# Kernel optimization log

Hardware: AMD Instinct MI355X
Metric: run time of the kernel (lower is better)

## Reference

```python
import jax, jax.numpy as jnp
import numpy as np

N = 100000
E = 1600000
D_IN = 50
D_H = 128
D_OUT = 128
EPS = 1e-5


def setup_inputs() -> dict:
    key = jax.random.key(0)
    ks = jax.random.split(key, 24)
    def w(k, shape, fan_in):
        return jax.random.normal(k, shape, jnp.float32) / np.sqrt(fan_in)
    inp = {
        'x': jax.random.normal(ks[0], (N, D_IN), jnp.float32),
        'edge_src': jax.random.randint(ks[1], (E,), 0, N, jnp.int32),
        'edge_dst': jax.random.randint(ks[2], (E,), 0, N, jnp.int32),
        # SAGEConv 1: D_IN -> D_H
        'Wl1': w(ks[3], (D_IN, D_H), D_IN), 'Wr1': w(ks[4], (D_IN, D_H), D_IN), 'b1': jnp.zeros((D_H,), jnp.float32),
        # SAGEConv 2: D_H -> D_H
        'Wl2': w(ks[5], (D_H, D_H), D_H), 'Wr2': w(ks[6], (D_H, D_H), D_H), 'b2': jnp.zeros((D_H,), jnp.float32),
        # SAGEConv 3: D_H -> D_OUT
        'Wl3': w(ks[7], (D_H, D_OUT), D_H), 'Wr3': w(ks[8], (D_H, D_OUT), D_H), 'b3': jnp.zeros((D_OUT,), jnp.float32),
        # skip linears (no bias)
        'Ws1': w(ks[9], (D_IN, D_H), D_IN), 'Ws2': w(ks[10], (D_IN, D_H), D_IN),
        # LayerNorm affine
        'lnw1': jnp.ones((D_H,), jnp.float32), 'lnb1': jnp.zeros((D_H,), jnp.float32),
        'lnw2': jnp.ones((D_H,), jnp.float32), 'lnb2': jnp.zeros((D_H,), jnp.float32),
        'lnw3': jnp.ones((D_OUT,), jnp.float32), 'lnb3': jnp.zeros((D_OUT,), jnp.float32),
        # PReLU scalar slopes (PyG init 0.25)
        'a1': jnp.float32(0.25), 'a2': jnp.float32(0.25), 'a3': jnp.float32(0.25),
    }
    return inp


def _sage(x, src, dst, Wl, Wr, b):
    # mean aggregation of source features at destinations, then linear + root
    msg = x[src]                                              # [E, d]
    agg = jax.ops.segment_sum(msg, dst, num_segments=N)       # [N, d]
    cnt = jax.ops.segment_sum(jnp.ones((src.shape[0],), x.dtype), dst, num_segments=N)
    mean = agg / jnp.maximum(cnt, 1.0)[:, None]
    return mean @ Wl + x @ Wr + b


def _graph_ln(x, w, b):
    # PyG LayerNorm mode='graph', batch=None: normalize over all nodes+channels
    xc = x - jnp.mean(x)
    std = jnp.sqrt(jnp.mean(xc * xc))
    return (xc / (std + EPS)) * w + b


def _prelu(x, a):
    return jnp.where(x >= 0, x, a * x)


def reference(x, edge_src, edge_dst, Wl1, Wr1, b1, Wl2, Wr2, b2, Wl3, Wr3, b3,
              Ws1, Ws2, lnw1, lnb1, lnw2, lnb2, lnw3, lnb3, a1, a2, a3):
    h1 = _sage(x, edge_src, edge_dst, Wl1, Wr1, b1)
    h1 = _prelu(_graph_ln(h1, lnw1, lnb1), a1)
    h2 = _sage(h1 + x @ Ws1, edge_src, edge_dst, Wl2, Wr2, b2)
    h2 = _prelu(_graph_ln(h2, lnw2, lnb2), a2)
    ret = _sage(h1 + h2 + x @ Ws2, edge_src, edge_dst, Wl3, Wr3, b3)
    ret = _prelu(_graph_ln(ret, lnw3, lnb3), a3)
    return ret
```

## Files before the change

kernel.cpp:

```cpp
#include <hip/hip_runtime.h>

#define D_IN 50
#define LN_EPS 1e-5f
#define BSH 8
#define MAXB 512

typedef __bf16 bf16_t;
typedef bf16_t bf16x8 __attribute__((ext_vector_type(8)));
typedef bf16_t bf16x4 __attribute__((ext_vector_type(4)));
typedef bf16_t bf16x2 __attribute__((ext_vector_type(2)));
typedef float f32x4_t __attribute__((ext_vector_type(4)));
typedef float f32x2_t __attribute__((ext_vector_type(2)));

#define ACCP(r, A)                                                            \
    {                                                                         \
        A[0] += (f32x2_t){__uint_as_float((r).x << 16),                       \
                          __uint_as_float((r).x & 0xffff0000u)};              \
        A[1] += (f32x2_t){__uint_as_float((r).y << 16),                       \
                          __uint_as_float((r).y & 0xffff0000u)};              \
        A[2] += (f32x2_t){__uint_as_float((r).z << 16),                       \
                          __uint_as_float((r).z & 0xffff0000u)};              \
        A[3] += (f32x2_t){__uint_as_float((r).w << 16),                       \
                          __uint_as_float((r).w & 0xffff0000u)};              \
    }

__global__ void bucket_hist_k(const int* __restrict__ dst, int* __restrict__ bcnt,
                              int e, int nb) {
    __shared__ int lh[MAXB];
    int t = threadIdx.x;
    for (int i = t; i < nb; i += 256) lh[i] = 0;
    __syncthreads();
    for (int i = blockIdx.x * 256 + t; i < e; i += gridDim.x * 256)
        atomicAdd(&lh[dst[i] >> BSH], 1);
    __syncthreads();
    for (int i = t; i < nb; i += 256) {
        int c = lh[i];
        if (c) atomicAdd(&bcnt[i * 16], c);
    }
}

__global__ void bscan_k(const int* __restrict__ bcnt, int* __restrict__ boff,
                        int* __restrict__ bpos, int nb, int e) {
    __shared__ int l[MAXB];
    int t = threadIdx.x;
    l[t] = (t < nb) ? bcnt[t * 16] : 0;
    __syncthreads();
    for (int off = 1; off < MAXB; off <<= 1) {
        int v = (t >= off) ? l[t - off] : 0;
        __syncthreads();
        l[t] += v;
        __syncthreads();
    }
    int excl = (t > 0) ? l[t - 1] : 0;
    if (t < nb) { boff[t] = excl; bpos[t * 16] = excl; }
    if (t == 0) boff[nb] = e;
}

__global__ void scatter_k(const int* __restrict__ src, const int* __restrict__ dst,
                          int* __restrict__ bpos, unsigned* __restrict__ pool,
                          int e, int nb) {
    __shared__ int lh[MAXB];
    __shared__ int lcur[MAXB];
    int t = threadIdx.x;
    for (int i = t; i < nb; i += 256) lh[i] = 0;
    __syncthreads();
    int chunk = (e + gridDim.x - 1) / gridDim.x;
    int s = blockIdx.x * chunk;
    int en = min(e, s + chunk);
    for (int i = s + t; i < en; i += 256)
        atomicAdd(&lh[dst[i] >> BSH], 1);
    __syncthreads();
    for (int i = t; i < nb; i += 256) {
        int c = lh[i];
        lcur[i] = c ? atomicAdd(&bpos[i * 16], c) : 0;
    }
    __syncthreads();
    for (int i = s + t; i < en; i += 256) {
        int d = dst[i];
        int p = atomicAdd(&lcur[d >> BSH], 1);
        pool[p] = (unsigned)src[i] | ((unsigned)(d & 255) << 17);
    }
}

__global__ void nhist_cfill_k(const unsigned* __restrict__ pool, const int* __restrict__ boff,
                              int* __restrict__ rp, int* __restrict__ col, int n) {
    __shared__ int lc[256];
    __shared__ int ls[256];
    __shared__ int lpos[256];
    int b = blockIdx.x, t = threadIdx.x;
    lc[t] = 0;
    __syncthreads();
    int s = boff[b], e = boff[b + 1];
    for (int i = s + t; i < e; i += 256) atomicAdd(&lc[pool[i] >> 17], 1);
    __syncthreads();
    int v = lc[t];
    ls[t] = v;
    __syncthreads();
    for (int off = 1; off < 256; off <<= 1) {
        int x = (t >= off) ? ls[t - off] : 0;
        __syncthreads();
        ls[t] += x;
        __syncthreads();
    }
    int excl = ls[t] - v;
    int nd = (b << BSH) + t;
    if (nd < n) rp[nd] = s + excl;
    if (nd == n - 1) rp[n] = e;
    lpos[t] = s + excl;
    __syncthreads();
    for (int i = s + t; i < e; i += 256) {
        unsigned pk = pool[i];
        int slot = atomicAdd(&lpos[pk >> 17], 1);
        col[slot] = (int)(pk & 0x1FFFFu);
    }
}

struct ConvDesc { const float* w; bf16_t* o; int kin; int kpad; };
struct ConvArgs { ConvDesc d[8]; };

__global__ void conv_w_k(ConvArgs args) {
    ConvDesc d = args.d[blockIdx.y];
    int i = blockIdx.x * 256 + threadIdx.x;
    int tot = 128 * d.kpad;
    if (i >= tot) return;
    int n = i / d.kpad, k = i - n * d.kpad;
    float v = (k < d.kin) ? d.w[(size_t)k * 128 + n] : 0.f;
    d.o[i] = (bf16_t)v;
}

__global__ void conv_x_k(const float* __restrict__ x, bf16_t* __restrict__ xb, int n) {
    int i = blockIdx.x * 256 + threadIdx.x;
    if (i >= n * 64) return;
    int node = i >> 6, k = i & 63;
    xb[i] = (k < D_IN) ? (bf16_t)x[node * D_IN + k] : (bf16_t)0.f;
}

__global__ void agg_bf64_k(const bf16_t* __restrict__ feat, const int* __restrict__ rp,
                           const int* __restrict__ col, bf16_t* __restrict__ mean, int n) {
    int wid = (blockIdx.x * blockDim.x + threadIdx.x) >> 6;
    int lane = threadIdx.x & 63;
    if (wid >= n) return;
    int start = rp[wid], end = rp[wid + 1];
    int lc = lane & 7;
    int g = lane >> 3;
    f32x2_t accA[4], accB[4];
#pragma unroll
    for (int k = 0; k < 4; k++) { accA[k] = (f32x2_t){0.f, 0.f}; accB[k] = (f32x2_t){0.f, 0.f}; }
    int e = start + g;
    if (e + 8 < end) {
        int i0 = col[e], i1 = col[e + 8];
        for (; e + 24 < end; e += 16) {
            uint4 r0 = *(const uint4*)(feat + (size_t)i0 * 64 + lc * 8);
            uint4 r1 = *(const uint4*)(feat + (size_t)i1 * 64 + lc * 8);
            i0 = col[e + 16];
            i1 = col[e + 24];
            ACCP(r0, accA);
            ACCP(r1, accB);
        }
        uint4 r0 = *(const uint4*)(feat + (size_t)i0 * 64 + lc * 8);
        uint4 r1 = *(const uint4*)(feat + (size_t)i1 * 64 + lc * 8);
        ACCP(r0, accA);
        ACCP(r1, accB);
        e += 16;
    }
    for (; e < end; e += 8) {
        uint4 r0 = *(const uint4*)(feat + (size_t)col[e] * 64 + lc * 8);
        ACCP(r0, accA);
    }
#pragma unroll
    for (int k = 0; k < 4; k++) accA[k] += accB[k];
    float aL[4], aH[4];
#pragma unroll
    for (int k = 0; k < 4; k++) { aL[k] = accA[k].x; aH[k] = accA[k].y; }
#pragma unroll
    for (int off = 8; off < 64; off <<= 1) {
#pragma unroll
        for (int k = 0; k < 4; k++) {
            aL[k] += __shfl_xor(aL[k], off);
            aH[k] += __shfl_xor(aH[k], off);
        }
    }
    int c = end - start;
    float invc = 1.f / (float)(c > 0 ? c : 1);
    if (lane < 8) {
        bf16x8 o;
#pragma unroll
        for (int k = 0; k < 4; k++) {
            o[2 * k] = (bf16_t)(aL[k] * invc);
            o[2 * k + 1] = (bf16_t)(aH[k] * invc);
        }
        *(bf16x8*)(mean + (size_t)wid * 64 + lc * 8) = o;
    }
}

__global__ void agg_bf128_k(const bf16_t* __restrict__ feat, const int* __restrict__ rp,
                            const int* __restrict__ col, bf16_t* __restrict__ mean, int n) {
    int wid = (blockIdx.x * blockDim.x + threadIdx.x) >> 6;
    int lane = threadIdx.x & 63;
    if (wid >= n) return;
    int start = rp[wid], end = rp[wid + 1];
    int lc = lane & 15;
    int g = lane >> 4;
    const uint* fp = (const uint*)feat + lc * 4;
    f32x2_t accA[4], accB[4];
#pragma unroll
    for (int k = 0; k < 4; k++) { accA[k] = (f32x2_t){0.f, 0.f}; accB[k] = (f32x2_t){0.f, 0.f}; }
    int e = start + g;
    int ng = (e < end) ? (((end - 1 - e) >> 2) + 1) : 0;
    int it = 0;
    for (; it + 4 <= ng; it += 4, e += 16) {
        int a = col[e], b = col[e + 4], c = col[e + 8], d = col[e + 12];
        uint4 r0 = *(const uint4*)(fp + (size_t)a * 64);
        uint4 r1 = *(const uint4*)(fp + (size_t)b * 64);
        uint4 r2 = *(const uint4*)(fp + (size_t)c * 64);
        uint4 r3 = *(const uint4*)(fp + (size_t)d * 64);
        ACCP(r0, accA);
        ACCP(r1, accB);
        ACCP(r2, accA);
        ACCP(r3, accB);
    }
    int rem = ng - it;
    if (rem > 0) {
        int a = col[e];
        int b = (rem > 1) ? col[e + 4] : a;
        int c = (rem > 2) ? col[e + 8] : b;
        uint4 r0 = *(const uint4*)(fp + (size_t)a * 64);
        uint4 r1 = *(const uint4*)(fp + (size_t)b * 64);
        uint4 r2 = *(const uint4*)(fp + (size_t)c * 64);
        ACCP(r0, accA);
        if (rem > 1) ACCP(r1, accB);
        if (rem > 2) ACCP(r2, accA);
    }
#pragma unroll
    for (int k = 0; k < 4; k++) accA[k] += accB[k];
    float aL[4], aH[4];
#pragma unroll
    for (int k = 0; k < 4; k++) { aL[k] = accA[k].x; aH[k] = accA[k].y; }
#pragma unroll
    for (int off = 16; off < 64; off <<= 1) {
#pragma unroll
        for (int k = 0; k < 4; k++) {
            aL[k] += __shfl_xor(aL[k], off);
            aH[k] += __shfl_xor(aH[k], off);
        }
    }
    int c = end - start;
    float invc = 1.f / (float)(c > 0 ? c : 1);
    if (lane < 16) {
        bf16x8 o;
#pragma unroll
        for (int k = 0; k < 4; k++) {
            o[2 * k] = (bf16_t)(aL[k] * invc);
            o[2 * k + 1] = (bf16_t)(aH[k] * invc);
        }
        *(bf16x8*)(mean + (size_t)wid * 128 + lc * 8) = o;
    }
}

template <int KPAD, bool DUAL, bool ACC>
__global__ __launch_bounds__(256) void mfma_gemm_k(
    const bf16_t* __restrict__ A, const bf16_t* __restrict__ B,
    const bf16_t* __restrict__ WlT, const bf16_t* __restrict__ WrT,
    const float* __restrict__ bias,
    bf16_t* __restrict__ out, float2* __restrict__ partials, int M) {
    constexpr int KC = KPAD / 32;
    constexpr int WELE = 8 * KC * 64 * 8;
    __shared__ bf16_t lwl[WELE];
    __shared__ bf16_t lwr[DUAL ? WELE : 8];

    const int tid = threadIdx.x;
    for (int ch = tid; ch < 8 * KC * 64; ch += 256) {
        int nt = ch / (KC * 64);
        int rem = ch - nt * (KC * 64);
        int c = rem >> 6;
        int ln = rem & 63;
        int m = ln & 15, q = ln >> 4;
        size_t srcoff = (size_t)(nt * 16 + m) * KPAD + c * 32 + q * 8;
        *(bf16x8*)&lwl[ch * 8] = *(const bf16x8*)(WlT + srcoff);
        if (DUAL) *(bf16x8*)&lwr[ch * 8] = *(const bf16x8*)(WrT + srcoff);
    }
    __syncthreads();

    const int wid = blockIdx.x * 4 + (tid >> 6);
    const int lane = tid & 63;
    const int row0 = wid * 32;
    if (row0 >= M) return;
    const int m = lane & 15;
    const int q = lane >> 4;

    bf16x8 af[2][KC], bfr[DUAL ? 2 : 1][DUAL ? KC : 1];
#pragma unroll
    for (int s = 0; s < 2; s++) {
        const bf16_t* ar = A + (size_t)(row0 + s * 16 + m) * KPAD + q * 8;
#pragma unroll
        for (int c = 0; c < KC; c++) af[s][c] = *(const bf16x8*)(ar + c * 32);
        if (DUAL) {
            const bf16_t* br = B + (size_t)(row0 + s * 16 + m) * KPAD + q * 8;
#pragma unroll
            for (int c = 0; c < KC; c++) bfr[s][c] = *(const bf16x8*)(br + c * 32);
        }
    }

    float lsum = 0.f, lsum2 = 0.f;
#pragma unroll
    for (int nt = 0; nt < 8; nt++) {
        f32x4_t acc0 = {0.f, 0.f, 0.f, 0.f};
        f32x4_t acc1 = {0.f, 0.f, 0.f, 0.f};
#pragma unroll
        for (int c = 0; c < KC; c++) {
            bf16x8 w = *(const bf16x8*)&lwl[((nt * KC + c) * 64 + lane) * 8];
            acc0 = __builtin_amdgcn_mfma_f32_16x16x32_bf16(af[0][c], w, acc0, 0, 0, 0);
            acc1 = __builtin_amdgcn_mfma_f32_16x16x32_bf16(af[1][c], w, acc1, 0, 0, 0);
        }
        if (DUAL) {
#pragma unroll
            for (int c = 0; c < KC; c++) {
                bf16x8 w = *(const bf16x8*)&lwr[((nt * KC + c) * 64 + lane) * 8];
                acc0 = __builtin_amdgcn_mfma_f32_16x16x32_bf16(bfr[0][c], w, acc0, 0, 0, 0);
                acc1 = __builtin_amdgcn_mfma_f32_16x16x32_bf16(bfr[1][c], w, acc1, 0, 0, 0);
            }
        }
        float bv = bias ? bias[nt * 16 + m] : 0.f;
#pragma unroll
        for (int s = 0; s < 2; s++) {
            f32x4_t* ap = (s == 0) ? &acc0 : &acc1;
#pragma unroll
            for (int r = 0; r < 4; r++) {
                int row = row0 + s * 16 + q * 4 + r;
                if (row < M) {
                    float o = (*ap)[r] + bv;
                    out[(size_t)row * 128 + nt * 16 + m] = (bf16_t)o;
                    if (ACC) { lsum += o; lsum2 += o * o; }
                }
            }
        }
    }
    if (ACC) {
        for (int off = 32; off > 0; off >>= 1) {
            lsum += __shfl_down(lsum, off);
            lsum2 += __shfl_down(lsum2, off);
        }
        if (lane == 0) partials[wid] = make_float2(lsum, lsum2);
    }
}

__global__ __launch_bounds__(256) void mfma_gemm3_k(
    const bf16_t* __restrict__ A, const bf16_t* __restrict__ B,
    const bf16_t* __restrict__ WlT, const bf16_t* __restrict__ WrT,
    const bf16_t* __restrict__ Ws1T, const bf16_t* __restrict__ Ws2T,
    const float* __restrict__ bias,
    bf16_t* __restrict__ outP, bf16_t* __restrict__ outC1, bf16_t* __restrict__ outC2,
    float2* __restrict__ partials, int M) {
    constexpr int KC = 2;
    constexpr int WELE = 8 * KC * 64 * 8;
    __shared__ bf16_t lwl[WELE];
    __shared__ bf16_t lwr[WELE];
    __shared__ bf16_t ls1[WELE];
    __shared__ bf16_t ls2[WELE];

    const int tid = threadIdx.x;
    for (int ch = tid; ch < 8 * KC * 64; ch += 256) {
        int nt = ch / (KC * 64);
        int rem = ch - nt * (KC * 64);
        int c = rem >> 6;
        int ln = rem & 63;
        int m = ln & 15, q = ln >> 4;
        size_t srcoff = (size_t)(nt * 16 + m) * 64 + c * 32 + q * 8;
        *(bf16x8*)&lwl[ch * 8] = *(const bf16x8*)(WlT + srcoff);
        *(bf16x8*)&lwr[ch * 8] = *(const bf16x8*)(WrT + srcoff);
        *(bf16x8*)&ls1[ch * 8] = *(const bf16x8*)(Ws1T + srcoff);
        *(bf16x8*)&ls2[ch * 8] = *(const bf16x8*)(Ws2T + srcoff);
    }
    __syncthreads();

    const int wid = blockIdx.x * 4 + (tid >> 6);
    const int lane = tid & 63;
    const int row0 = wid * 32;
    if (row0 >= M) return;
    const int m = lane & 15;
    const int q = lane >> 4;

    bf16x8 af[2][KC], bfr[2][KC];
#pragma unroll
    for (int s = 0; s < 2; s++) {
        const bf16_t* ar = A + (size_t)(row0 + s * 16 + m) * 64 + q * 8;
        const bf16_t* br = B + (size_t)(row0 + s * 16 + m) * 64 + q * 8;
#pragma unroll
        for (int c = 0; c < KC; c++) {
            af[s][c] = *(const bf16x8*)(ar + c * 32);
            bfr[s][c] = *(const bf16x8*)(br + c * 32);
        }
    }

    float lsum = 0.f, lsum2 = 0.f;
#pragma unroll
    for (int nt = 0; nt < 8; nt++) {
        f32x4_t aP0 = {0.f, 0.f, 0.f, 0.f}, aP1 = {0.f, 0.f, 0.f, 0.f};
        f32x4_t a10 = {0.f, 0.f, 0.f, 0.f}, a11 = {0.f, 0.f, 0.f, 0.f};
        f32x4_t a20 = {0.f, 0.f, 0.f, 0.f}, a21 = {0.f, 0.f, 0.f, 0.f};
#pragma unroll
        for (int c = 0; c < KC; c++) {
            int wi = ((nt * KC + c) * 64 + lane) * 8;
            bf16x8 wl = *(const bf16x8*)&lwl[wi];
            bf16x8 wr = *(const bf16x8*)&lwr[wi];
            bf16x8 w1 = *(const bf16x8*)&ls1[wi];
            bf16x8 w2 = *(const bf16x8*)&ls2[wi];
            aP0 = __builtin_amdgcn_mfma_f32_16x16x32_bf16(af[0][c], wl, aP0, 0, 0, 0);
            aP1 = __builtin_amdgcn_mfma_f32_16x16x32_bf16(af[1][c], wl, aP1, 0, 0, 0);
            aP0 = __builtin_amdgcn_mfma_f32_16x16x32_bf16(bfr[0][c], wr, aP0, 0, 0, 0);
            aP1 = __builtin_amdgcn_mfma_f32_16x16x32_bf16(bfr[1][c], wr, aP1, 0, 0, 0);
            a10 = __builtin_amdgcn_mfma_f32_16x16x32_bf16(bfr[0][c], w1, a10, 0, 0, 0);
            a11 = __builtin_amdgcn_mfma_f32_16x16x32_bf16(bfr[1][c], w1, a11, 0, 0, 0);
            a20 = __builtin_amdgcn_mfma_f32_16x16x32_bf16(bfr[0][c], w2, a20, 0, 0, 0);
            a21 = __builtin_amdgcn_mfma_f32_16x16x32_bf16(bfr[1][c], w2, a21, 0, 0, 0);
        }
        float bv = bias[nt * 16 + m];
#pragma unroll
        for (int s = 0; s < 2; s++) {
            f32x4_t* pP = (s == 0) ? &aP0 : &aP1;
            f32x4_t* p1 = (s == 0) ? &a10 : &a11;
            f32x4_t* p2 = (s == 0) ? &a20 : &a21;
#pragma unroll
            for (int r = 0; r < 4; r++) {
                int row = row0 + s * 16 + q * 4 + r;
                if (row < M) {
                    float o = (*pP)[r] + bv;
                    size_t oi = (size_t)row * 128 + nt * 16 + m;
                    outP[oi] = (bf16_t)o;
                    outC1[oi] = (bf16_t)(*p1)[r];
                    outC2[oi] = (bf16_t)(*p2)[r];
                    lsum += o; lsum2 += o * o;
                }
            }
        }
    }
    for (int off = 32; off > 0; off >>= 1) {
        lsum += __shfl_down(lsum, off);
        lsum2 += __shfl_down(lsum2, off);
    }
    if (lane == 0) partials[wid] = make_float2(lsum, lsum2);
}

__global__ void reduce_partials_k(const float2* __restrict__ p, int n,
                                  double* __restrict__ outp) {
    __shared__ double s1[256], s2[256];
    int t = threadIdx.x;
    double a = 0.0, b = 0.0;
    for (int i = t; i < n; i += 256) { a += (double)p[i].x; b += (double)p[i].y; }
    s1[t] = a; s2[t] = b;
    __syncthreads();
    for (int off = 128; off > 0; off >>= 1) {
        if (t < off) { s1[t] += s1[t + off]; s2[t] += s2[t + off]; }
        __syncthreads();
    }
    if (t == 0) { outp[0] = s1[0]; outp[1] = s2[0]; }
}

template <int MODE>
__global__ void ln_prelu_k(const bf16_t* __restrict__ pre, const bf16_t* __restrict__ h1in,
                           const bf16_t* __restrict__ s,
                           const float* __restrict__ lnw, const float* __restrict__ lnb,
                           const float* __restrict__ a_ptr, const double* __restrict__ acc,
                           void* __restrict__ out0v, void* __restrict__ out1v, int total) {
    int i = blockIdx.x * blockDim.x + threadIdx.x;
    if (i * 8 >= total) return;
    double cinv = 1.0 / (double)total;
    double mm = acc[0] * cinv;
    double var = acc[1] * cinv - mm * mm;
    float stdv = (float)sqrt(var > 0.0 ? var : 0.0);
    float scale = 1.0f / (stdv + LN_EPS);
    float mf = (float)mm;
    float a = a_ptr[0];
    int c8 = i & 15;
    float4 w0 = ((const float4*)lnw)[c8 * 2];
    float4 w1 = ((const float4*)lnw)[c8 * 2 + 1];
    float4 b0 = ((const float4*)lnb)[c8 * 2];
    float4 b1 = ((const float4*)lnb)[c8 * 2 + 1];
    float wv[8] = {w0.x, w0.y, w0.z, w0.w, w1.x, w1.y, w1.z, w1.w};
    float bv[8] = {b0.x, b0.y, b0.z, b0.w, b1.x, b1.y, b1.z, b1.w};
    bf16x8 p8 = ((const bf16x8*)pre)[i];
    float h[8];
#pragma unroll
    for (int k = 0; k < 8; k++) {
        float v = ((float)p8[k] - mf) * scale * wv[k] + bv[k];
        h[k] = v >= 0.f ? v : a * v;
    }
    if (MODE == 1) {
        bf16x8 hb, tb;
        bf16x8 sv = ((const bf16x8*)s)[i];
#pragma unroll
        for (int k = 0; k < 8; k++) {
            hb[k] = (bf16_t)h[k];
            tb[k] = (bf16_t)(h[k] + (float)sv[k]);
        }
        ((bf16x8*)out0v)[i] = hb;
        ((bf16x8*)out1v)[i] = tb;
    } else if (MODE == 2) {
        bf16x8 hv = ((const bf16x8*)h1in)[i];
        bf16x8 sv = ((const bf16x8*)s)[i];
        bf16x8 tb;
#pragma unroll
        for (int k = 0; k < 8; k++)
            tb[k] = (bf16_t)((float)hv[k] + h[k] + (float)sv[k]);
        ((bf16x8*)out0v)[i] = tb;
    } else {
        float4 o0 = {h[0], h[1], h[2], h[3]};
        float4 o1 = {h[4], h[5], h[6], h[7]};
        ((float4*)out0v)[i * 2] = o0;
        ((float4*)out0v)[i * 2 + 1] = o1;
    }
}

extern "C" void kernel_launch(void* const* d_in, const int* in_sizes, int n_in,
                              void* d_out, int out_size, void* d_ws, size_t ws_size,
                              hipStream_t stream) {
    const float* x    = (const float*)d_in[0];
    const int*   esrc = (const int*)d_in[1];
    const int*   edst = (const int*)d_in[2];
    const float* Wl1  = (const float*)d_in[3];
    const float* Wr1  = (const float*)d_in[4];
    const float* b1   = (const float*)d_in[5];
    const float* Wl2  = (const float*)d_in[6];
    const float* Wr2  = (const float*)d_in[7];
    const float* b2   = (const float*)d_in[8];
    const float* Wl3  = (const float*)d_in[9];
    const float* Wr3  = (const float*)d_in[10];
    const float* b3   = (const float*)d_in[11];
    const float* Ws1  = (const float*)d_in[12];
    const float* Ws2  = (const float*)d_in[13];
    const float* lnw1 = (const float*)d_in[14];
    const float* lnb1 = (const float*)d_in[15];
    const float* lnw2 = (const float*)d_in[16];
    const float* lnb2 = (const float*)d_in[17];
    const float* lnw3 = (const float*)d_in[18];
    const float* lnb3 = (const float*)d_in[19];
    const float* a1   = (const float*)d_in[20];
    const float* a2   = (const float*)d_in[21];
    const float* a3   = (const float*)d_in[22];

    const int N = in_sizes[0] / D_IN;
    const int E = in_sizes[1];
    const int NB = (N + 255) >> BSH;

    char* ws = (char*)d_ws;
    size_t off = 0;
    auto alloc = [&](size_t bytes) -> void* {
        void* p = ws + off;
        off += (bytes + 255) & ~(size_t)255;
        return p;
    };
    bf16_t* xb   = (bf16_t*)alloc((size_t)N * 64 * 2);
    bf16_t* mean = (bf16_t*)alloc((size_t)N * 128 * 2);
    bf16_t* PRE  = (bf16_t*)alloc((size_t)N * 128 * 2);
    bf16_t* C1   = (bf16_t*)alloc((size_t)N * 128 * 2);
    bf16_t* C2   = (bf16_t*)alloc((size_t)N * 128 * 2);
    bf16_t* h1b  = (bf16_t*)alloc((size_t)N * 128 * 2);
    bf16_t* TB   = (bf16_t*)alloc((size_t)N * 128 * 2);
    bf16_t* WT   = (bf16_t*)alloc((size_t)(4 * 128 * 64 + 4 * 128 * 128) * 2);
    int* rp   = (int*)alloc((size_t)(N + 1) * 4);
    int* col  = (int*)alloc((size_t)E * 4);
    int* bcnt = (int*)alloc((size_t)MAXB * 16 * 4);
    int* boff = (int*)alloc((size_t)(MAXB + 1) * 4);
    int* bpos = (int*)alloc((size_t)MAXB * 16 * 4);
    unsigned* pool = (unsigned*)alloc((size_t)E * 4);
    double* lnacc = (double*)alloc(6 * 8);
    const int tiles = (N + 31) / 32;
    float2* partials = (float2*)alloc((size_t)tiles * 8);

    bf16_t* Wl1T = WT;
    bf16_t* Wr1T = Wl1T + 128 * 64;
    bf16_t* Ws1T = Wr1T + 128 * 64;
    bf16_t* Ws2T = Ws1T + 128 * 64;
    bf16_t* Wl2T = Ws2T + 128 * 64;
    bf16_t* Wr2T = Wl2T + 128 * 128;
    bf16_t* Wl3T = Wr2T + 128 * 128;
    bf16_t* Wr3T = Wl3T + 128 * 128;

    hipMemsetAsync(bcnt, 0, (size_t)MAXB * 16 * 4, stream);

    bucket_hist_k<<<256, 256, 0, stream>>>(edst, bcnt, E, NB);
    bscan_k<<<1, MAXB, 0, stream>>>(bcnt, boff, bpos, NB, E);
    scatter_k<<<256, 256, 0, stream>>>(esrc, edst, bpos, pool, E, NB);
    nhist_cfill_k<<<NB, 256, 0, stream>>>(pool, boff, rp, col, N);

    ConvArgs ca;
    ca.d[0] = {Wl1, Wl1T, 50, 64};
    ca.d[1] = {Wr1, Wr1T, 50, 64};
    ca.d[2] = {Ws1, Ws1T, 50, 64};
    ca.d[3] = {Ws2, Ws2T, 50, 64};
    ca.d[4] = {Wl2, Wl2T, 128, 128};
    ca.d[5] = {Wr2, Wr2T, 128, 128};
    ca.d[6] = {Wl3, Wl3T, 128, 128};
    ca.d[7] = {Wr3, Wr3T, 128, 128};
    conv_w_k<<<dim3(64, 8), 256, 0, stream>>>(ca);
    conv_x_k<<<(N * 64 + 255) / 256, 256, 0, stream>>>(x, xb, N);

    const int aggBlocks = ((N * 64) + 255) / 256;
    const int gemmBlocks = (tiles + 3) / 4;
    const int lnBlocks = (N * 128 / 8 + 255) / 256;
    const int total = N * 128;

    agg_bf64_k<<<aggBlocks, 256, 0, stream>>>(xb, rp, col, mean, N);
    mfma_gemm3_k<<<gemmBlocks, 256, 0, stream>>>(
        mean, xb, Wl1T, Wr1T, Ws1T, Ws2T, b1, PRE, C1, C2, partials, N);
    reduce_partials_k<<<1, 256, 0, stream>>>(partials, tiles, lnacc + 0);
    ln_prelu_k<1><<<lnBlocks, 256, 0, stream>>>(
        PRE, nullptr, C1, lnw1, lnb1, a1, lnacc + 0, h1b, TB, total);

    agg_bf128_k<<<aggBlocks, 256, 0, stream>>>(TB, rp, col, mean, N);
    mfma_gemm_k<128, true, true><<<gemmBlocks, 256, 0, stream>>>(
        mean, TB, Wl2T, Wr2T, b2, PRE, partials, N);
    reduce_partials_k<<<1, 256, 0, stream>>>(partials, tiles, lnacc + 2);
    ln_prelu_k<2><<<lnBlocks, 256, 0, stream>>>(
        PRE, h1b, C2, lnw2, lnb2, a2, lnacc + 2, TB, nullptr, total);

    agg_bf128_k<<<aggBlocks, 256, 0, stream>>>(TB, rp, col, mean, N);
    mfma_gemm_k<128, true, true><<<gemmBlocks, 256, 0, stream>>>(
        mean, TB, Wl3T, Wr3T, b3, PRE, partials, N);
    reduce_partials_k<<<1, 256, 0, stream>>>(partials, tiles, lnacc + 4);
    ln_prelu_k<3><<<lnBlocks, 256, 0, stream>>>(
        PRE, nullptr, nullptr, lnw3, lnb3, a3, lnacc + 4, d_out, nullptr, total);
}
```

Before: 538.1 us.

## Fuse neighbor aggregation into MFMA GEMM and reduce LN stats via atomics

Merges the mean-aggregation kernels with the SAGE GEMM kernels. Each wave aggregates 16 nodes into shared memory and then runs MFMA on that tile, so the mean buffer is never written to or read back from global memory. LayerNorm partial sums are now added straight into double accumulators with atomics, which removes the reduce_partials kernels; the accumulators are zeroed inside the histogram kernel. Weights are read directly from global memory (L1/L2) rather than staged in LDS. The trade-offs are less parallelism per node during aggregation, since each wave processes 16 nodes in sequence, and more weight traffic per tile.

```diff
diff --git a/kernel.cpp b/kernel.cpp
--- a/kernel.cpp
+++ b/kernel.cpp
@@ -8,7 +8,6 @@
 typedef __bf16 bf16_t;
 typedef bf16_t bf16x8 __attribute__((ext_vector_type(8)));
 typedef bf16_t bf16x4 __attribute__((ext_vector_type(4)));
-typedef bf16_t bf16x2 __attribute__((ext_vector_type(2)));
 typedef float f32x4_t __attribute__((ext_vector_type(4)));
 typedef float f32x2_t __attribute__((ext_vector_type(2)));
 
@@ -25,9 +24,10 @@
     }
 
 __global__ void bucket_hist_k(const int* __restrict__ dst, int* __restrict__ bcnt,
-                              int e, int nb) {
+                              double* __restrict__ lnacc, int e, int nb) {
     __shared__ int lh[MAXB];
     int t = threadIdx.x;
+    if (blockIdx.x == 0 && t < 6) lnacc[t] = 0.0;
     for (int i = t; i < nb; i += 256) lh[i] = 0;
     __syncthreads();
     for (int i = blockIdx.x * 256 + t; i < e; i += gridDim.x * 256)
@@ -135,325 +135,211 @@
     xb[i] = (k < D_IN) ? (bf16_t)x[node * D_IN + k] : (bf16_t)0.f;
 }
 
-__global__ void agg_bf64_k(const bf16_t* __restrict__ feat, const int* __restrict__ rp,
-                           const int* __restrict__ col, bf16_t* __restrict__ mean, int n) {
-    int wid = (blockIdx.x * blockDim.x + threadIdx.x) >> 6;
-    int lane = threadIdx.x & 63;
-    if (wid >= n) return;
-    int start = rp[wid], end = rp[wid + 1];
-    int lc = lane & 7;
-    int g = lane >> 3;
-    f32x2_t accA[4], accB[4];
-#pragma unroll
-    for (int k = 0; k < 4; k++) { accA[k] = (f32x2_t){0.f, 0.f}; accB[k] = (f32x2_t){0.f, 0.f}; }
-    int e = start + g;
-    if (e + 8 < end) {
-        int i0 = col[e], i1 = col[e + 8];
-        for (; e + 24 < end; e += 16) {
-            uint4 r0 = *(const uint4*)(feat + (size_t)i0 * 64 + lc * 8);
-            uint4 r1 = *(const uint4*)(feat + (size_t)i1 * 64 + lc * 8);
-            i0 = col[e + 16];
-            i1 = col[e + 24];
-            ACCP(r0, accA);
-            ACCP(r1, accB);
-        }
-        uint4 r0 = *(const uint4*)(feat + (size_t)i0 * 64 + lc * 8);
-        uint4 r1 = *(const uint4*)(feat + (size_t)i1 * 64 + lc * 8);
-        ACCP(r0, accA);
-        ACCP(r1, accB);
-        e += 16;
-    }
-    for (; e < end; e += 8) {
-        uint4 r0 = *(const uint4*)(feat + (size_t)col[e] * 64 + lc * 8);
-        ACCP(r0, accA);
-    }
-#pragma unroll
-    for (int k = 0; k < 4; k++) accA[k] += accB[k];
-    float aL[4], aH[4];
-#pragma unroll
-    for (int k = 0; k < 4; k++) { aL[k] = accA[k].x; aH[k] = accA[k].y; }
-#pragma unroll
-    for (int off = 8; off < 64; off <<= 1) {
-#pragma unroll
-        for (int k = 0; k < 4; k++) {
-            aL[k] += __shfl_xor(aL[k], off);
-            aH[k] += __shfl_xor(aH[k], off);
-        }
-    }
-    int c = end - start;
-    float invc = 1.f / (float)(c > 0 ? c : 1);
-    if (lane < 8) {
-        bf16x8 o;
-#pragma unroll
-        for (int k = 0; k < 4; k++) {
-            o[2 * k] = (bf16_t)(aL[k] * invc);
-            o[2 * k + 1] = (bf16_t)(aH[k] * invc);
-        }
-        *(bf16x8*)(mean + (size_t)wid * 64 + lc * 8) = o;
-    }
-}
-
-__global__ void agg_bf128_k(const bf16_t* __restrict__ feat, const int* __restrict__ rp,
-                            const int* __restrict__ col, bf16_t* __restrict__ mean, int n) {
-    int wid = (blockIdx.x * blockDim.x + threadIdx.x) >> 6;
-    int lane = threadIdx.x & 63;
-    if (wid >= n) return;
-    int start = rp[wid], end = rp[wid + 1];
-    int lc = lane & 15;
-    int g = lane >> 4;
-    const uint* fp = (const uint*)feat + lc * 4;
-    f32x2_t accA[4], accB[4];
-#pragma unroll
-    for (int k = 0; k < 4; k++) { accA[k] = (f32x2_t){0.f, 0.f}; accB[k] = (f32x2_t){0.f, 0.f}; }
-    int e = start + g;
-    int ng = (e < end) ? (((end - 1 - e) >> 2) + 1) : 0;
-    int it = 0;
-    for (; it + 4 <= ng; it += 4, e += 16) {
-        int a = col[e], b = col[e + 4], c = col[e + 8], d = col[e + 12];
-        uint4 r0 = *(const uint4*)(fp + (size_t)a * 64);
-        uint4 r1 = *(const uint4*)(fp + (size_t)b * 64);
-        uint4 r2 = *(const uint4*)(fp + (size_t)c * 64);
-        uint4 r3 = *(const uint4*)(fp + (size_t)d * 64);
-        ACCP(r0, accA);
-        ACCP(r1, accB);
-        ACCP(r2, accA);
-        ACCP(r3, accB);
-    }
-    int rem = ng - it;
-    if (rem > 0) {
-        int a = col[e];
-        int b = (rem > 1) ? col[e + 4] : a;
-        int c = (rem > 2) ? col[e + 8] : b;
-        uint4 r0 = *(const uint4*)(fp + (size_t)a * 64);
-        uint4 r1 = *(const uint4*)(fp + (size_t)b * 64);
-        uint4 r2 = *(const uint4*)(fp + (size_t)c * 64);
-        ACCP(r0, accA);
-        if (rem > 1) ACCP(r1, accB);
-        if (rem > 2) ACCP(r2, accA);
-    }
-#pragma unroll
-    for (int k = 0; k < 4; k++) accA[k] += accB[k];
-    float aL[4], aH[4];
-#pragma unroll
-    for (int k = 0; k < 4; k++) { aL[k] = accA[k].x; aH[k] = accA[k].y; }
-#pragma unroll
-    for (int off = 16; off < 64; off <<= 1) {
-#pragma unroll
-        for (int k = 0; k < 4; k++) {
-            aL[k] += __shfl_xor(aL[k], off);
-            aH[k] += __shfl_xor(aH[k], off);
-        }
-    }
-    int c = end - start;
-    float invc = 1.f / (float)(c > 0 ? c : 1);
-    if (lane < 16) {
-        bf16x8 o;
-#pragma unroll
-        for (int k = 0; k < 4; k++) {
-            o[2 * k] = (bf16_t)(aL[k] * invc);
-            o[2 * k + 1] = (bf16_t)(aH[k] * invc);
-        }
-        *(bf16x8*)(mean + (size_t)wid * 128 + lc * 8) = o;
-    }
-}
-
-template <int KPAD, bool DUAL, bool ACC>
-__global__ __launch_bounds__(256) void mfma_gemm_k(
-    const bf16_t* __restrict__ A, const bf16_t* __restrict__ B,
-    const bf16_t* __restrict__ WlT, const bf16_t* __restrict__ WrT,
-    const float* __restrict__ bias,
-    bf16_t* __restrict__ out, float2* __restrict__ partials, int M) {
-    constexpr int KC = KPAD / 32;
-    constexpr int WELE = 8 * KC * 64 * 8;
-    __shared__ bf16_t lwl[WELE];
-    __shared__ bf16_t lwr[DUAL ? WELE : 8];
-
-    const int tid = threadIdx.x;
-    for (int ch = tid; ch < 8 * KC * 64; ch += 256) {
-        int nt = ch / (KC * 64);
-        int rem = ch - nt * (KC * 64);
-        int c = rem >> 6;
-        int ln = rem & 63;
-        int m = ln & 15, q = ln >> 4;
-        size_t srcoff = (size_t)(nt * 16 + m) * KPAD + c * 32 + q * 8;
-        *(bf16x8*)&lwl[ch * 8] = *(const bf16x8*)(WlT + srcoff);
-        if (DUAL) *(bf16x8*)&lwr[ch * 8] = *(const bf16x8*)(WrT + srcoff);
-    }
-    __syncthreads();
-
-    const int wid = blockIdx.x * 4 + (tid >> 6);
-    const int lane = tid & 63;
-    const int row0 = wid * 32;
-    if (row0 >= M) return;
-    const int m = lane & 15;
-    const int q = lane >> 4;
-
-    bf16x8 af[2][KC], bfr[DUAL ? 2 : 1][DUAL ? KC : 1];
-#pragma unroll
-    for (int s = 0; s < 2; s++) {
-        const bf16_t* ar = A + (size_t)(row0 + s * 16 + m) * KPAD + q * 8;
-#pragma unroll
-        for (int c = 0; c < KC; c++) af[s][c] = *(const bf16x8*)(ar + c * 32);
-        if (DUAL) {
-            const bf16_t* br = B + (size_t)(row0 + s * 16 + m) * KPAD + q * 8;
-#pragma unroll
-            for (int c = 0; c < KC; c++) bfr[s][c] = *(const bf16x8*)(br + c * 32);
-        }
-    }
-
-    float lsum = 0.f, lsum2 = 0.f;
-#pragma unroll
-    for (int nt = 0; nt < 8; nt++) {
-        f32x4_t acc0 = {0.f, 0.f, 0.f, 0.f};
-        f32x4_t acc1 = {0.f, 0.f, 0.f, 0.f};
-#pragma unroll
-        for (int c = 0; c < KC; c++) {
-            bf16x8 w = *(const bf16x8*)&lwl[((nt * KC + c) * 64 + lane) * 8];
-            acc0 = __builtin_amdgcn_mfma_f32_16x16x32_bf16(af[0][c], w, acc0, 0, 0, 0);
-            acc1 = __builtin_amdgcn_mfma_f32_16x16x32_bf16(af[1][c], w, acc1, 0, 0, 0);
-        }
-        if (DUAL) {
-#pragma unroll
-            for (int c = 0; c < KC; c++) {
-                bf16x8 w = *(const bf16x8*)&lwr[((nt * KC + c) * 64 + lane) * 8];
-                acc0 = __builtin_amdgcn_mfma_f32_16x16x32_bf16(bfr[0][c], w, acc0, 0, 0, 0);
-                acc1 = __builtin_amdgcn_mfma_f32_16x16x32_bf16(bfr[1][c], w, acc1, 0, 0, 0);
-            }
-        }
-        float bv = bias ? bias[nt * 16 + m] : 0.f;
-#pragma unroll
-        for (int s = 0; s < 2; s++) {
-            f32x4_t* ap = (s == 0) ? &acc0 : &acc1;
-#pragma unroll
-            for (int r = 0; r < 4; r++) {
-                int row = row0 + s * 16 + q * 4 + r;
-                if (row < M) {
-                    float o = (*ap)[r] + bv;
-                    out[(size_t)row * 128 + nt * 16 + m] = (bf16_t)o;
-                    if (ACC) { lsum += o; lsum2 += o * o; }
-                }
-            }
-        }
-    }
-    if (ACC) {
-        for (int off = 32; off > 0; off >>= 1) {
-            lsum += __shfl_down(lsum, off);
-            lsum2 += __shfl_down(lsum2, off);
-        }
-        if (lane == 0) partials[wid] = make_float2(lsum, lsum2);
-    }
-}
-
-__global__ __launch_bounds__(256) void mfma_gemm3_k(
-    const bf16_t* __restrict__ A, const bf16_t* __restrict__ B,
+template <int KPAD, bool TRIPLE>
+__global__ __launch_bounds__(256, 4) void agg_gemm_k(
+    const bf16_t* __restrict__ feat,
+    const int* __restrict__ rp, const int* __restrict__ col,
+    const bf16_t* __restrict__ B,
     const bf16_t* __restrict__ WlT, const bf16_t* __restrict__ WrT,
     const bf16_t* __restrict__ Ws1T, const bf16_t* __restrict__ Ws2T,
     const float* __restrict__ bias,
     bf16_t* __restrict__ outP, bf16_t* __restrict__ outC1, bf16_t* __restrict__ outC2,
-    float2* __restrict__ partials, int M) {
-    constexpr int KC = 2;
-    constexpr int WELE = 8 * KC * 64 * 8;
-    __shared__ bf16_t lwl[WELE];
-    __shared__ bf16_t lwr[WELE];
-    __shared__ bf16_t ls1[WELE];
-    __shared__ bf16_t ls2[WELE];
+    double* __restrict__ lnacc, int M) {
+    constexpr int KC = KPAD / 32;
+    __shared__ bf16_t lA[4][16][KPAD + 8];
+    __shared__ float rsum[4], rsum2[4];
 
     const int tid = threadIdx.x;
-    for (int ch = tid; ch < 8 * KC * 64; ch += 256) {
-        int nt = ch / (KC * 64);
-        int rem = ch - nt * (KC * 64);
-        int c = rem >> 6;
-        int ln = rem & 63;
-        int m = ln & 15, q = ln >> 4;
-        size_t srcoff = (size_t)(nt * 16 + m) * 64 + c * 32 + q * 8;
-        *(bf16x8*)&lwl[ch * 8] = *(const bf16x8*)(WlT + srcoff);
-        *(bf16x8*)&lwr[ch * 8] = *(const bf16x8*)(WrT + srcoff);
-        *(bf16x8*)&ls1[ch * 8] = *(const bf16x8*)(Ws1T + srcoff);
-        *(bf16x8*)&ls2[ch * 8] = *(const bf16x8*)(Ws2T + srcoff);
-    }
-    __syncthreads();
-
-    const int wid = blockIdx.x * 4 + (tid >> 6);
+    const int w = tid >> 6;
     const int lane = tid & 63;
-    const int row0 = wid * 32;
-    if (row0 >= M) return;
+    const int row0 = (blockIdx.x * 4 + w) * 16;
+
+    if (KPAD == 128) {
+        const int lc = lane & 15;
+        const int g = lane >> 4;
+        const uint* fp = (const uint*)feat + lc * 4;
+        for (int nd = 0; nd < 16; nd++) {
+            int node = row0 + nd;
+            f32x2_t accA[4], accB[4];
+#pragma unroll
+            for (int k = 0; k < 4; k++) { accA[k] = (f32x2_t){0.f, 0.f}; accB[k] = (f32x2_t){0.f, 0.f}; }
+            int cnt = 1;
+            if (node < M) {
+                int start = rp[node], end = rp[node + 1];
+                cnt = (end - start > 0) ? (end - start) : 1;
+                int e = start + g;
+                int ng = (e < end) ? (((end - 1 - e) >> 2) + 1) : 0;
+                int it = 0;
+                for (; it + 4 <= ng; it += 4, e += 16) {
+                    int a = col[e], b = col[e + 4], c = col[e + 8], d = col[e + 12];
+                    uint4 r0 = *(const uint4*)(fp + (size_t)a * 64);
+                    uint4 r1 = *(const uint4*)(fp + (size_t)b * 64);
+                    uint4 r2 = *(const uint4*)(fp + (size_t)c * 64);
+                    uint4 r3 = *(const uint4*)(fp + (size_t)d * 64);
+                    ACCP(r0, accA);
+                    ACCP(r1, accB);
+                    ACCP(r2, accA);
+                    ACCP(r3, accB);
+                }
+                int rem = ng - it;
+                if (rem > 0) {
+                    int a = col[e];
+                    int b = (rem > 1) ? col[e + 4] : a;
+                    int c = (rem > 2) ? col[e + 8] : b;
+                    uint4 r0 = *(const uint4*)(fp + (size_t)a * 64);
+                    uint4 r1 = *(const uint4*)(fp + (size_t)b * 64);
+                    uint4 r2 = *(const uint4*)(fp + (size_t)c * 64);
+                    ACCP(r0, accA);
+                    if (rem > 1) ACCP(r1, accB);
+                    if (rem > 2) ACCP(r2, accA);
+                }
+            }
+#pragma unroll
+            for (int k = 0; k < 4; k++) accA[k] += accB[k];
+            float aL[4], aH[4];
+#pragma unroll
+            for (int k = 0; k < 4; k++) { aL[k] = accA[k].x; aH[k] = accA[k].y; }
+#pragma unroll
+            for (int off = 16; off < 64; off <<= 1) {
+#pragma unroll
+                for (int k = 0; k < 4; k++) {
+                    aL[k] += __shfl_xor(aL[k], off);
+                    aH[k] += __shfl_xor(aH[k], off);
+                }
+            }
+            float invc = 1.f / (float)cnt;
+            if (lane < 16) {
+                bf16x8 o;
+#pragma unroll
+                for (int k = 0; k < 4; k++) {
+                    o[2 * k] = (bf16_t)(aL[k] * invc);
+                    o[2 * k + 1] = (bf16_t)(aH[k] * invc);
+                }
+                *(bf16x8*)&lA[w][nd][lc * 8] = o;
+            }
+        }
+    } else {
+        const int lc = lane & 7;
+        const int g = lane >> 3;
+        const uint* fp = (const uint*)feat + lc * 4;
+        for (int nd = 0; nd < 16; nd++) {
+            int node = row0 + nd;
+            f32x2_t accA[4], accB[4];
+#pragma unroll
+            for (int k = 0; k < 4; k++) { accA[k] = (f32x2_t){0.f, 0.f}; accB[k] = (f32x2_t){0.f, 0.f}; }
+            int cnt = 1;
+            if (node < M) {
+                int start = rp[node], end = rp[node + 1];
+                cnt = (end - start > 0) ? (end - start) : 1;
+                int e = start + g;
+                if (e + 8 < end) {
+                    int i0 = col[e], i1 = col[e + 8];
+                    for (; e + 24 < end; e += 16) {
+                        uint4 r0 = *(const uint4*)(fp + (size_t)i0 * 32);
+                        uint4 r1 = *(const uint4*)(fp + (size_t)i1 * 32);
+                        i0 = col[e + 16];
+                        i1 = col[e + 24];
+                        ACCP(r0, accA);
+                        ACCP(r1, accB);
+                    }
+                    uint4 r0 = *(const uint4*)(fp + (size_t)i0 * 32);
+                    uint4 r1 = *(const uint4*)(fp + (size_t)i1 * 32);
+                    ACCP(r0, accA);
+                    ACCP(r1, accB);
+                    e += 16;
+                }
+                for (; e < end; e += 8) {
+                    uint4 r0 = *(const uint4*)(fp + (size_t)col[e] * 32);
+                    ACCP(r0, accA);
+                }
+            }
+#pragma unroll
+            for (int k = 0; k < 4; k++) accA[k] += accB[k];
+            float aL[4], aH[4];
+#pragma unroll
+            for (int k = 0; k < 4; k++) { aL[k] = accA[k].x; aH[k] = accA[k].y; }
+#pragma unroll
+            for (int off = 8; off < 64; off <<= 1) {
+#pragma unroll
+                for (int k = 0; k < 4; k++) {
+                    aL[k] += __shfl_xor(aL[k], off);
+                    aH[k] += __shfl_xor(aH[k], off);
+                }
+            }
+            float invc = 1.f / (float)cnt;
+            if (lane < 8) {
+                bf16x8 o;
+#pragma unroll
+                for (int k = 0; k < 4; k++) {
+                    o[2 * k] = (bf16_t)(aL[k] * invc);
+                    o[2 * k + 1] = (bf16_t)(aH[k] * invc);
+                }
+                *(bf16x8*)&lA[w][nd][lc * 8] = o;
+            }
+        }
+    }
+
     const int m = lane & 15;
     const int q = lane >> 4;
 
-    bf16x8 af[2][KC], bfr[2][KC];
-#pragma unroll
-    for (int s = 0; s < 2; s++) {
-        const bf16_t* ar = A + (size_t)(row0 + s * 16 + m) * 64 + q * 8;
-        const bf16_t* br = B + (size_t)(row0 + s * 16 + m) * 64 + q * 8;
+    bf16x8 af[KC], bfr[KC];
+#pragma unroll
+    for (int c = 0; c < KC; c++) af[c] = *(const bf16x8*)&lA[w][m][q * 8 + c * 32];
+    {
+        const bf16_t* br = B + (size_t)(row0 + m) * KPAD + q * 8;
+#pragma unroll
+        for (int c = 0; c < KC; c++) bfr[c] = *(const bf16x8*)(br + c * 32);
+    }
+
+    float lsum = 0.f, lsum2 = 0.f;
+#pragma unroll 2
+    for (int nt = 0; nt < 8; nt++) {
+        f32x4_t aP = {0.f, 0.f, 0.f, 0.f};
+        f32x4_t a1 = {0.f, 0.f, 0.f, 0.f};
+        f32x4_t a2 = {0.f, 0.f, 0.f, 0.f};
 #pragma unroll
         for (int c = 0; c < KC; c++) {
-            af[s][c] = *(const bf16x8*)(ar + c * 32);
-            bfr[s][c] = *(const bf16x8*)(br + c * 32);
-        }
-    }
-
-    float lsum = 0.f, lsum2 = 0.f;
-#pragma unroll
-    for (int nt = 0; nt < 8; nt++) {
-        f32x4_t aP0 = {0.f, 0.f, 0.f, 0.f}, aP1 = {0.f, 0.f, 0.f, 0.f};
-        f32x4_t a10 = {0.f, 0.f, 0.f, 0.f}, a11 = {0.f, 0.f, 0.f, 0.f};
-        f32x4_t a20 = {0.f, 0.f, 0.f, 0.f}, a21 = {0.f, 0.f, 0.f, 0.f};
-#pragma unroll
-        for (int c = 0; c < KC; c++) {
-            int wi = ((nt * KC + c) * 64 + lane) * 8;
-            bf16x8 wl = *(const bf16x8*)&lwl[wi];
-            bf16x8 wr = *(const bf16x8*)&lwr[wi];
-            bf16x8 w1 = *(const bf16x8*)&ls1[wi];
-            bf16x8 w2 = *(const bf16x8*)&ls2[wi];
-            aP0 = __builtin_amdgcn_mfma_f32_16x16x32_bf16(af[0][c], wl, aP0, 0, 0, 0);
-            aP1 = __builtin_amdgcn_mfma_f32_16x16x32_bf16(af[1][c], wl, aP1, 0, 0, 0);
-            aP0 = __builtin_amdgcn_mfma_f32_16x16x32_bf16(bfr[0][c], wr, aP0, 0, 0, 0);
-            aP1 = __builtin_amdgcn_mfma_f32_16x16x32_bf16(bfr[1][c], wr, aP1, 0, 0, 0);
-            a10 = __builtin_amdgcn_mfma_f32_16x16x32_bf16(bfr[0][c], w1, a10, 0, 0, 0);
-            a11 = __builtin_amdgcn_mfma_f32_16x16x32_bf16(bfr[1][c], w1, a11, 0, 0, 0);
-            a20 = __builtin_amdgcn_mfma_f32_16x16x32_bf16(bfr[0][c], w2, a20, 0, 0, 0);
-            a21 = __builtin_amdgcn_mfma_f32_16x16x32_bf16(bfr[1][c], w2, a21, 0, 0, 0);
+            size_t woff = (size_t)(nt * 16 + m) * KPAD + c * 32 + q * 8;
+            bf16x8 wl = *(const bf16x8*)(WlT + woff);
+            bf16x8 wr = *(const bf16x8*)(WrT + woff);
+            aP = __builtin_amdgcn_mfma_f32_16x16x32_bf16(af[c], wl, aP, 0, 0, 0);
+            aP = __builtin_amdgcn_mfma_f32_16x16x32_bf16(bfr[c], wr, aP, 0, 0, 0);
+            if (TRIPLE) {
+                bf16x8 w1 = *(const bf16x8*)(Ws1T + woff);
+                bf16x8 w2 = *(const bf16x8*)(Ws2T + woff);
+                a1 = __builtin_amdgcn_mfma_f32_16x16x32_bf16(bfr[c], w1, a1, 0, 0, 0);
+                a2 = __builtin_amdgcn_mfma_f32_16x16x32_bf16(bfr[c], w2, a2, 0, 0, 0);
+            }
         }
         float bv = bias[nt * 16 + m];
 #pragma unroll
-        for (int s = 0; s < 2; s++) {
-            f32x4_t* pP = (s == 0) ? &aP0 : &aP1;
-            f32x4_t* p1 = (s == 0) ? &a10 : &a11;
-            f32x4_t* p2 = (s == 0) ? &a20 : &a21;
-#pragma unroll
-            for (int r = 0; r < 4; r++) {
-                int row = row0 + s * 16 + q * 4 + r;
-                if (row < M) {
-                    float o = (*pP)[r] + bv;
-                    size_t oi = (size_t)row * 128 + nt * 16 + m;
-                    outP[oi] = (bf16_t)o;
-                    outC1[oi] = (bf16_t)(*p1)[r];
-                    outC2[oi] = (bf16_t)(*p2)[r];
-                    lsum += o; lsum2 += o * o;
+        for (int r = 0; r < 4; r++) {
+            int row = row0 + q * 4 + r;
+            if (row < M) {
+                float o = aP[r] + bv;
+                size_t oi = (size_t)row * 128 + nt * 16 + m;
+                outP[oi] = (bf16_t)o;
+                lsum += o; lsum2 += o * o;
+                if (TRIPLE) {
+                    outC1[oi] = (bf16_t)a1[r];
+                    outC2[oi] = (bf16_t)a2[r];
                 }
             }
         }
     }
+
     for (int off = 32; off > 0; off >>= 1) {
         lsum += __shfl_down(lsum, off);
         lsum2 += __shfl_down(lsum2, off);
     }
-    if (lane == 0) partials[wid] = make_float2(lsum, lsum2);
-}
-
-__global__ void reduce_partials_k(const float2* __restrict__ p, int n,
-                                  double* __restrict__ outp) {
-    __shared__ double s1[256], s2[256];
-    int t = threadIdx.x;
-    double a = 0.0, b = 0.0;
-    for (int i = t; i < n; i += 256) { a += (double)p[i].x; b += (double)p[i].y; }
-    s1[t] = a; s2[t] = b;
-    __syncthreads();
-    for (int off = 128; off > 0; off >>= 1) {
-        if (t < off) { s1[t] += s1[t + off]; s2[t] += s2[t + off]; }
-        __syncthreads();
-    }
-    if (t == 0) { outp[0] = s1[0]; outp[1] = s2[0]; }
+    if (lane == 0) { rsum[w] = lsum; rsum2[w] = lsum2; }
+    __syncthreads();
+    if (tid == 0) {
+        double s = (double)rsum[0] + (double)rsum[1] + (double)rsum[2] + (double)rsum[3];
+        double s2 = (double)rsum2[0] + (double)rsum2[1] + (double)rsum2[2] + (double)rsum2[3];
+        unsafeAtomicAdd(&lnacc[0], s);
+        unsafeAtomicAdd(&lnacc[1], s2);
+    }
 }
 
 template <int MODE>
@@ -550,7 +436,6 @@
         return p;
     };
     bf16_t* xb   = (bf16_t*)alloc((size_t)N * 64 * 2);
-    bf16_t* mean = (bf16_t*)alloc((size_t)N * 128 * 2);
     bf16_t* PRE  = (bf16_t*)alloc((size_t)N * 128 * 2);
     bf16_t* C1   = (bf16_t*)alloc((size_t)N * 128 * 2);
     bf16_t* C2   = (bf16_t*)alloc((size_t)N * 128 * 2);
@@ -564,8 +449,6 @@
     int* bpos = (int*)alloc((size_t)MAXB * 16 * 4);
     unsigned* pool = (unsigned*)alloc((size_t)E * 4);
     double* lnacc = (double*)alloc(6 * 8);
-    const int tiles = (N + 31) / 32;
-    float2* partials = (float2*)alloc((size_t)tiles * 8);
 
     bf16_t* Wl1T = WT;
     bf16_t* Wr1T = Wl1T + 128 * 64;
@@ -578,7 +461,7 @@
 
     hipMemsetAsync(bcnt, 0, (size_t)MAXB * 16 * 4, stream);
 
-    bucket_hist_k<<<256, 256, 0, stream>>>(edst, bcnt, E, NB);
+    bucket_hist_k<<<256, 256, 0, stream>>>(edst, bcnt, lnacc, E, NB);
     bscan_k<<<1, MAXB, 0, stream>>>(bcnt, boff, bpos, NB, E);
     scatter_k<<<256, 256, 0, stream>>>(esrc, edst, bpos, pool, E, NB);
     nhist_cfill_k<<<NB, 256, 0, stream>>>(pool, boff, rp, col, N);
@@ -595,29 +478,24 @@
     conv_w_k<<<dim3(64, 8), 256, 0, stream>>>(ca);
     conv_x_k<<<(N * 64 + 255) / 256, 256, 0, stream>>>(x, xb, N);
 
-    const int aggBlocks = ((N * 64) + 255) / 256;
-    const int gemmBlocks = (tiles + 3) / 4;
+    const int fusedBlocks = (N + 63) / 64;
     const int lnBlocks = (N * 128 / 8 + 255) / 256;
     const int total = N * 128;
 
-    agg_bf64_k<<<aggBlocks, 256, 0, stream>>>(xb, rp, col, mean, N);
-    mfma_gemm3_k<<<gemmBlocks, 256, 0, stream>>>(
-        mean, xb, Wl1T, Wr1T, Ws1T, Ws2T, b1, PRE, C1, C2, partials, N);
-    reduce_partials_k<<<1, 256, 0, stream>>>(partials, tiles, lnacc + 0);
+    agg_gemm_k<64, true><<<fusedBlocks, 256, 0, stream>>>(
+        xb, rp, col, xb, Wl1T, Wr1T, Ws1T, Ws2T, b1, PRE, C1, C2, lnacc + 0, N);
     ln_prelu_k<1><<<lnBlocks, 256, 0, stream>>>(
         PRE, nullptr, C1, lnw1, lnb1, a1, lnacc + 0, h1b, TB, total);
 
-    agg_bf128_k<<<aggBlocks, 256, 0, stream>>>(TB, rp, col, mean, N);
-    mfma_gemm_k<128, true, true><<<gemmBlocks, 256, 0, stream>>>(
-        mean, TB, Wl2T, Wr2T, b2, PRE, partials, N);
-    reduce_partials_k<<<1, 256, 0, stream>>>(partials, tiles, lnacc + 2);
+    agg_gemm_k<128, false><<<fusedBlocks, 256, 0, stream>>>(
+        TB, rp, col, TB, Wl2T, Wr2T, nullptr, nullptr, b2, PRE, nullptr, nullptr,
+        lnacc + 2, N);
     ln_prelu_k<2><<<lnBlocks, 256, 0, stream>>>(
         PRE, h1b, C2, lnw2, lnb2, a2, lnacc + 2, TB, nullptr, total);
 
-    agg_bf128_k<<<aggBlocks, 256, 0, stream>>>(TB, rp, col, mean, N);
-    mfma_gemm_k<128, true, true><<<gemmBlocks, 256, 0, stream>>>(
-        mean, TB, Wl3T, Wr3T, b3, PRE, partials, N);
-    reduce_partials_k<<<1, 256, 0, stream>>>(partials, tiles, lnacc + 4);
+    agg_gemm_k<128, false><<<fusedBlocks, 256, 0, stream>>>(
+        TB, rp, col, TB, Wl3T, Wr3T, nullptr, nullptr, b3, PRE, nullptr, nullptr,
+        lnacc + 4, N);
     ln_prelu_k<3><<<lnBlocks, 256, 0, stream>>>(
         PRE, nullptr, nullptr, lnw3, lnb3, a3, lnacc + 4, d_out, nullptr, total);
 }
```

Result: slower. 636.8 us (+18.4%).
